# Kernel tuning notes

Hardware: AMD Instinct MI355X
Metric: run time of the kernel (lower is better)

The kernel has to match this reference:

```python
import jax, jax.numpy as jnp
import numpy as np

T, B, I, H, O = 512, 64, 512, 1024, 512
STDV = 1.0 / np.sqrt(H)


def setup_inputs() -> dict:
    key = jax.random.key(0)
    ks = jax.random.split(key, 12)
    u = lambda k, shape: jax.random.uniform(k, shape, jnp.float32, -STDV, STDV)
    return {
        "input": jax.random.normal(ks[0], (T, B, I), jnp.float32),
        "state": jnp.zeros((B, H), jnp.float32),
        "W_zh": u(ks[1], (H, H)), "W_zx": u(ks[2], (I, H)), "b_z": u(ks[3], (H,)),
        "W_rh": u(ks[4], (H, H)), "W_rx": u(ks[5], (I, H)), "b_r": u(ks[6], (H,)),
        "W_hh": u(ks[7], (H, H)), "W_hx": u(ks[8], (I, H)), "b_h": u(ks[9], (H,)),
        "W_out": u(ks[10], (O, H)), "b_out": u(ks[11], (O,)),
    }


def reference(input, state, W_zh, W_zx, b_z, W_rh, W_rx, b_r, W_hh, W_hx, b_h, W_out, b_out):
    # input: [T, B, I]; state: [B, H]
    def step(h, x):
        z = jax.nn.sigmoid(h @ W_zh + x @ W_zx + b_z)
        r = jax.nn.sigmoid(h @ W_rh + x @ W_rx + b_r)
        ht = jnp.tanh((h * r) @ W_hh + x @ W_hx + b_h)
        h = (1.0 - z) * h + z * ht
        y = h @ W_out.T + b_out  # Linear(hidim -> outdim)
        return h, y

    h_final, Y = jax.lax.scan(step, state, input)  # Y: [T, B, O]
    # torch.cat(Y, dim=0) -> [T*B, O]
    return Y.reshape(T * B, O), h_final
```

## Files before the change

kernel.cpp:

```cpp
#include <hip/hip_runtime.h>
#include <cstdint>


#define TT 512
#define BB 64
#define II 512
#define HH 1024
#define OO 512
#define NTHR 512
#define NBLK 512

typedef float4 f4;
__device__ __forceinline__ f4 ld4(const float* p){ return *reinterpret_cast<const f4*>(p); }
__device__ __forceinline__ int swz(int k){ return k ^ (((k >> 4) & 7) << 2); }

__device__ __forceinline__ void ldc16(const float* p, f4* d){
  asm volatile(
    "global_load_dwordx4 %0,  %16, off sc0 sc1\n\t"
    "global_load_dwordx4 %1,  %16, off offset:256 sc0 sc1\n\t"
    "global_load_dwordx4 %2,  %16, off offset:512 sc0 sc1\n\t"
    "global_load_dwordx4 %3,  %16, off offset:768 sc0 sc1\n\t"
    "global_load_dwordx4 %4,  %16, off offset:1024 sc0 sc1\n\t"
    "global_load_dwordx4 %5,  %16, off offset:1280 sc0 sc1\n\t"
    "global_load_dwordx4 %6,  %16, off offset:1536 sc0 sc1\n\t"
    "global_load_dwordx4 %7,  %16, off offset:1792 sc0 sc1\n\t"
    "global_load_dwordx4 %8,  %16, off offset:2048 sc0 sc1\n\t"
    "global_load_dwordx4 %9,  %16, off offset:2304 sc0 sc1\n\t"
    "global_load_dwordx4 %10, %16, off offset:2560 sc0 sc1\n\t"
    "global_load_dwordx4 %11, %16, off offset:2816 sc0 sc1\n\t"
    "global_load_dwordx4 %12, %16, off offset:3072 sc0 sc1\n\t"
    "global_load_dwordx4 %13, %16, off offset:3328 sc0 sc1\n\t"
    "global_load_dwordx4 %14, %16, off offset:3584 sc0 sc1\n\t"
    "s_waitcnt vmcnt(1)\n\t"
    "global_load_dwordx4 %15, %16, off offset:3840 sc0 sc1\n\t"
    "s_waitcnt vmcnt(0)"
    : "=&v"(d[0]),"=&v"(d[1]),"=&v"(d[2]),"=&v"(d[3]),
      "=&v"(d[4]),"=&v"(d[5]),"=&v"(d[6]),"=&v"(d[7]),
      "=&v"(d[8]),"=&v"(d[9]),"=&v"(d[10]),"=&v"(d[11]),
      "=&v"(d[12]),"=&v"(d[13]),"=&v"(d[14]),"=&v"(d[15])
    : "v"(p) : "memory");
}
__device__ __forceinline__ float ldc1(const float* p){
  float v;
  asm volatile("global_load_dword %0, %1, off sc0 sc1\n\ts_waitcnt vmcnt(0)"
               : "=v"(v) : "v"(p) : "memory");
  return v;
}
__device__ __forceinline__ void stc1(float* p, float v){
  asm volatile("global_store_dword %0, %1, off sc0 sc1" :: "v"(p), "v"(v) : "memory");
}

__global__ void k_transpose_x(const float* __restrict__ x, float* __restrict__ xT){
  size_t total = (size_t)TT * II * BB;
  for (size_t n = (size_t)blockIdx.x * blockDim.x + threadIdx.x; n < total;
       n += (size_t)gridDim.x * blockDim.x){
    size_t t = n / ((size_t)II * BB);
    size_t rem = n % ((size_t)II * BB);
    size_t i = rem / BB, b = rem % BB;
    xT[n] = x[(t * BB + b) * II + i];
  }
}

__global__ void k_transpose_wx(const float* __restrict__ W, float* __restrict__ WT){
  size_t n = (size_t)blockIdx.x * blockDim.x + threadIdx.x;
  if (n >= (size_t)II * HH) return;
  size_t j = n / II, k = n % II;
  WT[n] = W[k * HH + j];
}

__global__ void k_transpose_h0(const float* __restrict__ st, float* __restrict__ h0){
  size_t n = (size_t)blockIdx.x * blockDim.x + threadIdx.x;
  if (n >= (size_t)HH * BB) return;
  size_t j = n / BB, b = n % BB;
  h0[n] = st[b * HH + j];
}

__global__ void k_init_bars(unsigned* bars){
  if (threadIdx.x < 1024) bars[threadIdx.x] = 0;
}

__device__ __forceinline__ void g_arrive(unsigned* bars, int g, int jt, unsigned ep){
  asm volatile("s_waitcnt vmcnt(0)" ::: "memory");
  unsigned* leaf = bars + (g * 17 + (jt & 15)) * 16;
  unsigned old = __hip_atomic_fetch_add(leaf, 1u, __ATOMIC_RELAXED, __HIP_MEMORY_SCOPE_AGENT);
  if (old + 1u == ep * 16u)
    __hip_atomic_fetch_add(bars + (g * 17 + 16) * 16, 1u, __ATOMIC_RELAXED, __HIP_MEMORY_SCOPE_AGENT);
}
__device__ __forceinline__ void g_wait(unsigned* bars, int g, unsigned ep){
  unsigned* root = bars + (g * 17 + 16) * 16;
  while (__hip_atomic_load(root, __ATOMIC_RELAXED, __HIP_MEMORY_SCOPE_AGENT) < ep * 16u)
    __builtin_amdgcn_s_sleep(1);
}

#define WREDUCE(v) { v += __shfl_xor(v, 8); v += __shfl_xor(v, 16); v += __shfl_xor(v, 32); }

__global__ __launch_bounds__(NTHR, 2) void k_gru(
    const float* __restrict__ xT,
    const float* __restrict__ WxTr, const float* __restrict__ WxTz, const float* __restrict__ WxTh,
    float* __restrict__ h, float* __restrict__ s,
    const float* __restrict__ W_zh, const float* __restrict__ b_z,
    const float* __restrict__ W_rh, const float* __restrict__ b_r,
    const float* __restrict__ W_hh, const float* __restrict__ b_h,
    const float* __restrict__ W_out, const float* __restrict__ b_out,
    float* __restrict__ out, unsigned* __restrict__ bars)
{
  __shared__ float sW[3 * 4 * 1024];
  __shared__ float red[8 * 272];
  __shared__ float xpre[3][128];
  __shared__ float sZ[128];
  __shared__ float sBias[16];

  const int tid = threadIdx.x;
  const int bid = blockIdx.x;
  const int jt = bid & 255, bhalf = bid >> 8;
  const int j0 = jt * 4, o0 = jt * 2, bbase = bhalf * 32;

  #pragma unroll
  for (int kk2 = 0; kk2 < 2; ++kk2){
    const int k = tid * 2 + kk2;
    f4 vr = ld4(W_rh + (size_t)k * HH + j0);
    f4 vz = ld4(W_zh + (size_t)k * HH + j0);
    f4 vh = ld4(W_hh + (size_t)k * HH + j0);
    const int kx = swz(k);
    float ar[4] = {vr.x,vr.y,vr.z,vr.w};
    float az[4] = {vz.x,vz.y,vz.z,vz.w};
    float ah[4] = {vh.x,vh.y,vh.z,vh.w};
    #pragma unroll
    for (int c = 0; c < 4; ++c){
      sW[0*4096 + c*1024 + kx] = ar[c];
      sW[1*4096 + c*1024 + kx] = az[c];
      sW[2*4096 + c*1024 + kx] = ah[c];
    }
  }
  if (tid < 4){
    sBias[tid]     = b_r[j0 + tid];
    sBias[4 + tid] = b_z[j0 + tid];
    sBias[8 + tid] = b_h[j0 + tid];
    if (tid < 2) sBias[12 + tid] = b_out[o0 + tid];
  }

  const int bg = tid & 7, b0 = bbase + bg * 4;
  const int ksec = tid >> 3;
  const int wv = tid >> 6;
  const bool wr0 = ((tid & 56) == 0);
  const int kh0 = ksec * 16;
  const int kx0 = ksec * 8;
  __syncthreads();

  for (int t = -1; t < TT; ++t){
    f4 st4[16];
    if (t >= 0){
      float aR[4][4] = {};
      ldc16(h + kh0 * BB + b0, st4);
      #pragma unroll
      for (int i4 = 0; i4 < 4; ++i4){
        const int kxc = swz(kh0 + i4*4);
        #pragma unroll
        for (int c = 0; c < 4; ++c){
          f4 wf = *reinterpret_cast<const f4*>(&sW[0*4096 + c*1024 + kxc]);
          float wvv[4] = {wf.x, wf.y, wf.z, wf.w};
          #pragma unroll
          for (int kk = 0; kk < 4; ++kk){
            const f4 hv = st4[i4*4+kk];
            aR[c][0] = fmaf(wvv[kk], hv.x, aR[c][0]);
            aR[c][1] = fmaf(wvv[kk], hv.y, aR[c][1]);
            aR[c][2] = fmaf(wvv[kk], hv.z, aR[c][2]);
            aR[c][3] = fmaf(wvv[kk], hv.w, aR[c][3]);
          }
        }
      }
      #pragma unroll
      for (int c = 0; c < 4; ++c)
        #pragma unroll
        for (int bb = 0; bb < 4; ++bb) WREDUCE(aR[c][bb]);
      if (wr0)
        #pragma unroll
        for (int c = 0; c < 4; ++c)
          #pragma unroll
          for (int bb = 0; bb < 4; ++bb)
            red[wv*272 + c*32 + bg*4 + bb] = aR[c][bb];
      __syncthreads();
      if (tid < 128){
        float sum = 0.f;
        #pragma unroll
        for (int w = 0; w < 8; ++w) sum += red[w*272 + tid];
        const int c = tid >> 5, bl = tid & 31;
        const float v = sum + xpre[0][tid] + sBias[c];
        const float rr = 1.f / (1.f + expf(-v));
        const int jg = j0 + c, bgl = bbase + bl;
        stc1(&s[jg*BB + bgl], rr * ldc1(&h[jg*BB + bgl]));
      }
      __syncthreads();
      if (tid == 0) g_arrive(bars, bhalf, jt, 2*t + 1);

      float aZ[4][4] = {};
      float aY[2][4] = {};
      #pragma unroll
      for (int i4 = 0; i4 < 4; ++i4){
        const int kc = kh0 + i4*4;
        const int kxc = swz(kc);
        #pragma unroll
        for (int c = 0; c < 4; ++c){
          f4 wf = *reinterpret_cast<const f4*>(&sW[1*4096 + c*1024 + kxc]);
          float wvv[4] = {wf.x, wf.y, wf.z, wf.w};
          #pragma unroll
          for (int kk = 0; kk < 4; ++kk){
            const f4 hv = st4[i4*4+kk];
            aZ[c][0] = fmaf(wvv[kk], hv.x, aZ[c][0]);
            aZ[c][1] = fmaf(wvv[kk], hv.y, aZ[c][1]);
            aZ[c][2] = fmaf(wvv[kk], hv.z, aZ[c][2]);
            aZ[c][3] = fmaf(wvv[kk], hv.w, aZ[c][3]);
          }
        }
        #pragma unroll
        for (int oc = 0; oc < 2; ++oc){
          f4 wo = ld4(W_out + (size_t)(o0 + oc) * HH + kc);
          float wvv[4] = {wo.x, wo.y, wo.z, wo.w};
          #pragma unroll
          for (int kk = 0; kk < 4; ++kk){
            const f4 hv = st4[i4*4+kk];
            aY[oc][0] = fmaf(wvv[kk], hv.x, aY[oc][0]);
            aY[oc][1] = fmaf(wvv[kk], hv.y, aY[oc][1]);
            aY[oc][2] = fmaf(wvv[kk], hv.z, aY[oc][2]);
            aY[oc][3] = fmaf(wvv[kk], hv.w, aY[oc][3]);
          }
        }
      }
      #pragma unroll
      for (int c = 0; c < 4; ++c)
        #pragma unroll
        for (int bb = 0; bb < 4; ++bb) WREDUCE(aZ[c][bb]);
      #pragma unroll
      for (int oc = 0; oc < 2; ++oc)
        #pragma unroll
        for (int bb = 0; bb < 4; ++bb) WREDUCE(aY[oc][bb]);
      if (wr0){
        #pragma unroll
        for (int c = 0; c < 4; ++c)
          #pragma unroll
          for (int bb = 0; bb < 4; ++bb)
            red[wv*272 + c*32 + bg*4 + bb] = aZ[c][bb];
        #pragma unroll
        for (int oc = 0; oc < 2; ++oc)
          #pragma unroll
          for (int bb = 0; bb < 4; ++bb)
            red[wv*272 + 128 + oc*32 + bg*4 + bb] = aY[oc][bb];
      }
      __syncthreads();
      if (tid < 128){
        float sum = 0.f;
        #pragma unroll
        for (int w = 0; w < 8; ++w) sum += red[w*272 + tid];
        const int c = tid >> 5;
        sZ[tid] = 1.f / (1.f + expf(-(sum + xpre[1][tid] + sBias[4 + c])));
      } else if (tid < 192){
        const int idx = tid - 128;
        float sum = 0.f;
        #pragma unroll
        for (int w = 0; w < 8; ++w) sum += red[w*272 + tid];
        const int oc = idx >> 5, bl = idx & 31;
        if (t > 0)
          out[((size_t)(t-1)*BB + bbase + bl)*OO + o0 + oc] = sum + sBias[12 + oc];
      }
      if (tid == 0) g_wait(bars, bhalf, 2*t + 1);
      __syncthreads();

      float aH[4][4] = {};
      f4 sv16[16];
      ldc16(s + kh0 * BB + b0, sv16);
      #pragma unroll
      for (int i4 = 0; i4 < 4; ++i4){
        const int kxc = swz(kh0 + i4*4);
        #pragma unroll
        for (int c = 0; c < 4; ++c){
          f4 wf = *reinterpret_cast<const f4*>(&sW[2*4096 + c*1024 + kxc]);
          float wvv[4] = {wf.x, wf.y, wf.z, wf.w};
          #pragma unroll
          for (int kk = 0; kk < 4; ++kk){
            const f4 sv = sv16[i4*4+kk];
            aH[c][0] = fmaf(wvv[kk], sv.x, aH[c][0]);
            aH[c][1] = fmaf(wvv[kk], sv.y, aH[c][1]);
            aH[c][2] = fmaf(wvv[kk], sv.z, aH[c][2]);
            aH[c][3] = fmaf(wvv[kk], sv.w, aH[c][3]);
          }
        }
      }
      #pragma unroll
      for (int c = 0; c < 4; ++c)
        #pragma unroll
        for (int bb = 0; bb < 4; ++bb) WREDUCE(aH[c][bb]);
      if (wr0)
        #pragma unroll
        for (int c = 0; c < 4; ++c)
          #pragma unroll
          for (int bb = 0; bb < 4; ++bb)
            red[wv*272 + c*32 + bg*4 + bb] = aH[c][bb];
      __syncthreads();
      if (tid < 128){
        float sum = 0.f;
        #pragma unroll
        for (int w = 0; w < 8; ++w) sum += red[w*272 + tid];
        const int c = tid >> 5, bl = tid & 31;
        const int jg = j0 + c, bgl = bbase + bl;
        const float ht = tanhf(sum + xpre[2][tid] + sBias[8 + c]);
        const float z = sZ[tid];
        const float hold = ldc1(&h[jg*BB + bgl]);
        const float hnew = fmaf(z, ht - hold, hold);
        stc1(&h[jg*BB + bgl], hnew);
        if (t == TT - 1) out[(size_t)TT*BB*OO + (size_t)bgl*HH + jg] = hnew;
      }
      __syncthreads();
      if (tid == 0) g_arrive(bars, bhalf, jt, 2*t + 2);
    }

    if (t + 1 < TT){
      const int tc = t + 1;
      float aXr[4][4] = {}, aXz[4][4] = {}, aXh[4][4] = {};
      const float* xb = xT + (size_t)tc * II * BB + kx0 * BB + b0;
      #pragma unroll
      for (int i4 = 0; i4 < 2; ++i4){
        f4 xv4[4];
        #pragma unroll
        for (int kk = 0; kk < 4; ++kk) xv4[kk] = ld4(xb + (i4*4+kk) * BB);
        #pragma unroll
        for (int c = 0; c < 4; ++c){
          f4 wr_ = ld4(WxTr + (size_t)(j0 + c) * II + kx0 + i4*4);
          f4 wz_ = ld4(WxTz + (size_t)(j0 + c) * II + kx0 + i4*4);
          f4 wh_ = ld4(WxTh + (size_t)(j0 + c) * II + kx0 + i4*4);
          float wrv[4] = {wr_.x, wr_.y, wr_.z, wr_.w};
          float wzv[4] = {wz_.x, wz_.y, wz_.z, wz_.w};
          float whv[4] = {wh_.x, wh_.y, wh_.z, wh_.w};
          #pragma unroll
          for (int kk = 0; kk < 4; ++kk){
            const f4 xv = xv4[kk];
            aXr[c][0] = fmaf(wrv[kk], xv.x, aXr[c][0]);
            aXr[c][1] = fmaf(wrv[kk], xv.y, aXr[c][1]);
            aXr[c][2] = fmaf(wrv[kk], xv.z, aXr[c][2]);
            aXr[c][3] = fmaf(wrv[kk], xv.w, aXr[c][3]);
            aXz[c][0] = fmaf(wzv[kk], xv.x, aXz[c][0]);
            aXz[c][1] = fmaf(wzv[kk], xv.y, aXz[c][1]);
            aXz[c][2] = fmaf(wzv[kk], xv.z, aXz[c][2]);
            aXz[c][3] = fmaf(wzv[kk], xv.w, aXz[c][3]);
            aXh[c][0] = fmaf(whv[kk], xv.x, aXh[c][0]);
            aXh[c][1] = fmaf(whv[kk], xv.y, aXh[c][1]);
            aXh[c][2] = fmaf(whv[kk], xv.z, aXh[c][2]);
            aXh[c][3] = fmaf(whv[kk], xv.w, aXh[c][3]);
          }
        }
      }
      #pragma unroll
      for (int c = 0; c < 4; ++c)
        #pragma unroll
        for (int bb = 0; bb < 4; ++bb){ WREDUCE(aXr[c][bb]); WREDUCE(aXz[c][bb]); WREDUCE(aXh[c][bb]); }
      if (wr0)
        #pragma unroll
        for (int c = 0; c < 4; ++c)
          #pragma unroll
          for (int bb = 0; bb < 4; ++bb){
            red[wv*272 + c*32 + bg*4 + bb]       = aXr[c][bb];
            red[wv*272 + 128 + c*32 + bg*4 + bb] = aXz[c][bb];
          }
      __syncthreads();
      if (tid < 256){
        float sum = 0.f;
        #pragma unroll
        for (int w = 0; w < 8; ++w) sum += red[w*272 + tid];
        if (tid < 128) xpre[0][tid] = sum;
        else           xpre[1][tid - 128] = sum;
      }
      __syncthreads();
      if (wr0)
        #pragma unroll
        for (int c = 0; c < 4; ++c)
          #pragma unroll
          for (int bb = 0; bb < 4; ++bb)
            red[wv*272 + c*32 + bg*4 + bb] = aXh[c][bb];
      __syncthreads();
      if (tid < 128){
        float sum = 0.f;
        #pragma unroll
        for (int w = 0; w < 8; ++w) sum += red[w*272 + tid];
        xpre[2][tid] = sum;
      }
      __syncthreads();
    }

    if (t >= 0){
      if (tid == 0) g_wait(bars, bhalf, 2*t + 2);
      __syncthreads();
    }
  }

  {
    float aY[2][4] = {};
    f4 hv16[16];
    ldc16(h + kh0 * BB + b0, hv16);
    #pragma unroll
    for (int i4 = 0; i4 < 4; ++i4){
      const int kc = kh0 + i4*4;
      #pragma unroll
      for (int oc = 0; oc < 2; ++oc){
        f4 wo = ld4(W_out + (size_t)(o0 + oc) * HH + kc);
        float wvv[4] = {wo.x, wo.y, wo.z, wo.w};
        #pragma unroll
        for (int kk = 0; kk < 4; ++kk){
          const f4 hv = hv16[i4*4+kk];
          aY[oc][0] = fmaf(wvv[kk], hv.x, aY[oc][0]);
          aY[oc][1] = fmaf(wvv[kk], hv.y, aY[oc][1]);
          aY[oc][2] = fmaf(wvv[kk], hv.z, aY[oc][2]);
          aY[oc][3] = fmaf(wvv[kk], hv.w, aY[oc][3]);
        }
      }
    }
    #pragma unroll
    for (int oc = 0; oc < 2; ++oc)
      #pragma unroll
      for (int bb = 0; bb < 4; ++bb) WREDUCE(aY[oc][bb]);
    if (wr0)
      #pragma unroll
      for (int oc = 0; oc < 2; ++oc)
        #pragma unroll
        for (int bb = 0; bb < 4; ++bb)
          red[wv*272 + oc*32 + bg*4 + bb] = aY[oc][bb];
    __syncthreads();
    if (tid < 64){
      float sum = 0.f;
      #pragma unroll
      for (int w = 0; w < 8; ++w) sum += red[w*272 + tid];
      const int oc = tid >> 5, bl = tid & 31;
      out[((size_t)(TT-1)*BB + bbase + bl)*OO + o0 + oc] = sum + sBias[12 + oc];
    }
  }
}

extern "C" void kernel_launch(void* const* d_in, const int* in_sizes, int n_in,
                              void* d_out, int out_size, void* d_ws, size_t ws_size,
                              hipStream_t stream) {
  const float* x     = (const float*)d_in[0];
  const float* st    = (const float*)d_in[1];
  const float* W_zh  = (const float*)d_in[2];
  const float* W_zx  = (const float*)d_in[3];
  const float* b_z   = (const float*)d_in[4];
  const float* W_rh  = (const float*)d_in[5];
  const float* W_rx  = (const float*)d_in[6];
  const float* b_r   = (const float*)d_in[7];
  const float* W_hh  = (const float*)d_in[8];
  const float* W_hx  = (const float*)d_in[9];
  const float* b_h   = (const float*)d_in[10];
  const float* W_out = (const float*)d_in[11];
  const float* b_out = (const float*)d_in[12];
  float* out = (float*)d_out;
  float* ws  = (float*)d_ws;

  const size_t xT_sz = (size_t)TT * II * BB;
  const size_t wx_sz = (size_t)II * HH;
  const size_t h_sz  = (size_t)HH * BB;
  const size_t need  = (xT_sz + 3*wx_sz + 2*h_sz) * sizeof(float) + 1024*sizeof(unsigned);
  if (ws_size < need) return;

  float* xT   = ws;
  float* WxTr = xT + xT_sz;
  float* WxTz = WxTr + wx_sz;
  float* WxTh = WxTz + wx_sz;
  float* h    = WxTh + wx_sz;
  float* s    = h + h_sz;
  unsigned* bars = (unsigned*)(s + h_sz);

  k_transpose_x <<<8192, 256, 0, stream>>>(x, xT);
  k_transpose_wx<<<2048, 256, 0, stream>>>(W_rx, WxTr);
  k_transpose_wx<<<2048, 256, 0, stream>>>(W_zx, WxTz);
  k_transpose_wx<<<2048, 256, 0, stream>>>(W_hx, WxTh);
  k_transpose_h0<<< 256, 256, 0, stream>>>(st, h);
  k_init_bars   <<<   1, 1024, 0, stream>>>(bars);

  k_gru<<<NBLK, NTHR, 0, stream>>>(xT, WxTr, WxTz, WxTh, h, s,
                                   W_zh, b_z, W_rh, b_r, W_hh, b_h,
                                   W_out, b_out, out, bars);
}
```

Before: 15.05 ms.

## Merge batch halves into one 1024-thread block per hidden tile with single barrier group

Replaces the 512-block, 512-thread grid that split the batch into two halves with 256 blocks of 1024 threads, each covering all 64 batch columns for four hidden units. The two barrier trees collapse into a single grid barrier. The hidden-state loads are streamed in chunks of four instead of holding sixteen vectors, which lowers register pressure, and the input-projection accumulation runs one gate at a time. The aim is to halve the redundant weight staging and barrier traffic per step, at the cost of one block per CU with less latency hiding and a larger shared-memory reduction.

```diff
diff --git a/kernel.cpp b/kernel.cpp
--- a/kernel.cpp
+++ b/kernel.cpp
@@ -7,37 +7,22 @@
 #define II 512
 #define HH 1024
 #define OO 512
-#define NTHR 512
-#define NBLK 512
+#define NTHR 1024
+#define NBLK 256
+#define RSTR 528
 
 typedef float4 f4;
 __device__ __forceinline__ f4 ld4(const float* p){ return *reinterpret_cast<const f4*>(p); }
 __device__ __forceinline__ int swz(int k){ return k ^ (((k >> 4) & 7) << 2); }
 
-__device__ __forceinline__ void ldc16(const float* p, f4* d){
+__device__ __forceinline__ void ldc4(const float* p, f4* d){
   asm volatile(
-    "global_load_dwordx4 %0,  %16, off sc0 sc1\n\t"
-    "global_load_dwordx4 %1,  %16, off offset:256 sc0 sc1\n\t"
-    "global_load_dwordx4 %2,  %16, off offset:512 sc0 sc1\n\t"
-    "global_load_dwordx4 %3,  %16, off offset:768 sc0 sc1\n\t"
-    "global_load_dwordx4 %4,  %16, off offset:1024 sc0 sc1\n\t"
-    "global_load_dwordx4 %5,  %16, off offset:1280 sc0 sc1\n\t"
-    "global_load_dwordx4 %6,  %16, off offset:1536 sc0 sc1\n\t"
-    "global_load_dwordx4 %7,  %16, off offset:1792 sc0 sc1\n\t"
-    "global_load_dwordx4 %8,  %16, off offset:2048 sc0 sc1\n\t"
-    "global_load_dwordx4 %9,  %16, off offset:2304 sc0 sc1\n\t"
-    "global_load_dwordx4 %10, %16, off offset:2560 sc0 sc1\n\t"
-    "global_load_dwordx4 %11, %16, off offset:2816 sc0 sc1\n\t"
-    "global_load_dwordx4 %12, %16, off offset:3072 sc0 sc1\n\t"
-    "global_load_dwordx4 %13, %16, off offset:3328 sc0 sc1\n\t"
-    "global_load_dwordx4 %14, %16, off offset:3584 sc0 sc1\n\t"
-    "s_waitcnt vmcnt(1)\n\t"
-    "global_load_dwordx4 %15, %16, off offset:3840 sc0 sc1\n\t"
+    "global_load_dwordx4 %0, %4, off sc0 sc1\n\t"
+    "global_load_dwordx4 %1, %4, off offset:256 sc0 sc1\n\t"
+    "global_load_dwordx4 %2, %4, off offset:512 sc0 sc1\n\t"
+    "global_load_dwordx4 %3, %4, off offset:768 sc0 sc1\n\t"
     "s_waitcnt vmcnt(0)"
-    : "=&v"(d[0]),"=&v"(d[1]),"=&v"(d[2]),"=&v"(d[3]),
-      "=&v"(d[4]),"=&v"(d[5]),"=&v"(d[6]),"=&v"(d[7]),
-      "=&v"(d[8]),"=&v"(d[9]),"=&v"(d[10]),"=&v"(d[11]),
-      "=&v"(d[12]),"=&v"(d[13]),"=&v"(d[14]),"=&v"(d[15])
+    : "=&v"(d[0]),"=&v"(d[1]),"=&v"(d[2]),"=&v"(d[3])
     : "v"(p) : "memory");
 }
 __device__ __forceinline__ float ldc1(const float* p){
@@ -76,25 +61,24 @@
 }
 
 __global__ void k_init_bars(unsigned* bars){
-  if (threadIdx.x < 1024) bars[threadIdx.x] = 0;
-}
-
-__device__ __forceinline__ void g_arrive(unsigned* bars, int g, int jt, unsigned ep){
+  if (threadIdx.x < 512) bars[threadIdx.x] = 0;
+}
+
+__device__ __forceinline__ void g_arrive(unsigned* bars, int bid, unsigned ep){
   asm volatile("s_waitcnt vmcnt(0)" ::: "memory");
-  unsigned* leaf = bars + (g * 17 + (jt & 15)) * 16;
+  unsigned* leaf = bars + (bid & 15) * 16;
   unsigned old = __hip_atomic_fetch_add(leaf, 1u, __ATOMIC_RELAXED, __HIP_MEMORY_SCOPE_AGENT);
   if (old + 1u == ep * 16u)
-    __hip_atomic_fetch_add(bars + (g * 17 + 16) * 16, 1u, __ATOMIC_RELAXED, __HIP_MEMORY_SCOPE_AGENT);
-}
-__device__ __forceinline__ void g_wait(unsigned* bars, int g, unsigned ep){
-  unsigned* root = bars + (g * 17 + 16) * 16;
-  while (__hip_atomic_load(root, __ATOMIC_RELAXED, __HIP_MEMORY_SCOPE_AGENT) < ep * 16u)
+    __hip_atomic_fetch_add(bars + 256, 1u, __ATOMIC_RELAXED, __HIP_MEMORY_SCOPE_AGENT);
+}
+__device__ __forceinline__ void g_wait(unsigned* bars, unsigned ep){
+  while (__hip_atomic_load(bars + 256, __ATOMIC_RELAXED, __HIP_MEMORY_SCOPE_AGENT) < ep * 16u)
     __builtin_amdgcn_s_sleep(1);
 }
 
-#define WREDUCE(v) { v += __shfl_xor(v, 8); v += __shfl_xor(v, 16); v += __shfl_xor(v, 32); }
-
-__global__ __launch_bounds__(NTHR, 2) void k_gru(
+#define WREDUCE(v) { v += __shfl_xor(v, 16); v += __shfl_xor(v, 32); }
+
+__global__ __launch_bounds__(NTHR) void k_gru(
     const float* __restrict__ xT,
     const float* __restrict__ WxTr, const float* __restrict__ WxTz, const float* __restrict__ WxTh,
     float* __restrict__ h, float* __restrict__ s,
@@ -105,19 +89,17 @@
     float* __restrict__ out, unsigned* __restrict__ bars)
 {
   __shared__ float sW[3 * 4 * 1024];
-  __shared__ float red[8 * 272];
-  __shared__ float xpre[3][128];
-  __shared__ float sZ[128];
+  __shared__ float red[16 * RSTR];
+  __shared__ float xpre[3][256];
+  __shared__ float sZ[256];
   __shared__ float sBias[16];
 
   const int tid = threadIdx.x;
   const int bid = blockIdx.x;
-  const int jt = bid & 255, bhalf = bid >> 8;
-  const int j0 = jt * 4, o0 = jt * 2, bbase = bhalf * 32;
-
-  #pragma unroll
-  for (int kk2 = 0; kk2 < 2; ++kk2){
-    const int k = tid * 2 + kk2;
+  const int j0 = bid * 4, o0 = bid * 2;
+
+  {
+    const int k = tid;
     f4 vr = ld4(W_rh + (size_t)k * HH + j0);
     f4 vz = ld4(W_zh + (size_t)k * HH + j0);
     f4 vh = ld4(W_hh + (size_t)k * HH + j0);
@@ -139,264 +121,253 @@
     if (tid < 2) sBias[12 + tid] = b_out[o0 + tid];
   }
 
-  const int bg = tid & 7, b0 = bbase + bg * 4;
-  const int ksec = tid >> 3;
+  const int bg = tid & 15, b0 = bg * 4;
+  const int ksec = tid >> 4;
   const int wv = tid >> 6;
-  const bool wr0 = ((tid & 56) == 0);
+  const bool wr0 = ((tid & 48) == 0);
   const int kh0 = ksec * 16;
   const int kx0 = ksec * 8;
   __syncthreads();
 
   for (int t = -1; t < TT; ++t){
-    f4 st4[16];
     if (t >= 0){
-      float aR[4][4] = {};
-      ldc16(h + kh0 * BB + b0, st4);
-      #pragma unroll
-      for (int i4 = 0; i4 < 4; ++i4){
-        const int kxc = swz(kh0 + i4*4);
-        #pragma unroll
-        for (int c = 0; c < 4; ++c){
-          f4 wf = *reinterpret_cast<const f4*>(&sW[0*4096 + c*1024 + kxc]);
-          float wvv[4] = {wf.x, wf.y, wf.z, wf.w};
-          #pragma unroll
-          for (int kk = 0; kk < 4; ++kk){
-            const f4 hv = st4[i4*4+kk];
-            aR[c][0] = fmaf(wvv[kk], hv.x, aR[c][0]);
-            aR[c][1] = fmaf(wvv[kk], hv.y, aR[c][1]);
-            aR[c][2] = fmaf(wvv[kk], hv.z, aR[c][2]);
-            aR[c][3] = fmaf(wvv[kk], hv.w, aR[c][3]);
+      const float* hb = h + kh0 * BB + b0;
+
+      {
+        float aR[4][4] = {};
+        #pragma unroll
+        for (int i4 = 0; i4 < 4; ++i4){
+          f4 hv4[4];
+          ldc4(hb + i4*4*BB, hv4);
+          const int kxc = swz(kh0 + i4*4);
+          #pragma unroll
+          for (int c = 0; c < 4; ++c){
+            f4 wf = *reinterpret_cast<const f4*>(&sW[0*4096 + c*1024 + kxc]);
+            float wvv[4] = {wf.x, wf.y, wf.z, wf.w};
+            #pragma unroll
+            for (int kk = 0; kk < 4; ++kk){
+              const f4 hv = hv4[kk];
+              aR[c][0] = fmaf(wvv[kk], hv.x, aR[c][0]);
+              aR[c][1] = fmaf(wvv[kk], hv.y, aR[c][1]);
+              aR[c][2] = fmaf(wvv[kk], hv.z, aR[c][2]);
+              aR[c][3] = fmaf(wvv[kk], hv.w, aR[c][3]);
+            }
           }
         }
-      }
-      #pragma unroll
-      for (int c = 0; c < 4; ++c)
-        #pragma unroll
-        for (int bb = 0; bb < 4; ++bb) WREDUCE(aR[c][bb]);
-      if (wr0)
         #pragma unroll
         for (int c = 0; c < 4; ++c)
           #pragma unroll
-          for (int bb = 0; bb < 4; ++bb)
-            red[wv*272 + c*32 + bg*4 + bb] = aR[c][bb];
-      __syncthreads();
-      if (tid < 128){
+          for (int bb = 0; bb < 4; ++bb) WREDUCE(aR[c][bb]);
+        if (wr0)
+          #pragma unroll
+          for (int c = 0; c < 4; ++c)
+            #pragma unroll
+            for (int bb = 0; bb < 4; ++bb)
+              red[wv*RSTR + c*64 + b0 + bb] = aR[c][bb];
+      }
+      __syncthreads();
+      if (tid < 256){
         float sum = 0.f;
         #pragma unroll
-        for (int w = 0; w < 8; ++w) sum += red[w*272 + tid];
-        const int c = tid >> 5, bl = tid & 31;
+        for (int w = 0; w < 16; ++w) sum += red[w*RSTR + tid];
+        const int c = tid >> 6, bl = tid & 63;
         const float v = sum + xpre[0][tid] + sBias[c];
         const float rr = 1.f / (1.f + expf(-v));
-        const int jg = j0 + c, bgl = bbase + bl;
-        stc1(&s[jg*BB + bgl], rr * ldc1(&h[jg*BB + bgl]));
-      }
-      __syncthreads();
-      if (tid == 0) g_arrive(bars, bhalf, jt, 2*t + 1);
-
-      float aZ[4][4] = {};
-      float aY[2][4] = {};
-      #pragma unroll
-      for (int i4 = 0; i4 < 4; ++i4){
-        const int kc = kh0 + i4*4;
-        const int kxc = swz(kc);
-        #pragma unroll
-        for (int c = 0; c < 4; ++c){
-          f4 wf = *reinterpret_cast<const f4*>(&sW[1*4096 + c*1024 + kxc]);
-          float wvv[4] = {wf.x, wf.y, wf.z, wf.w};
-          #pragma unroll
-          for (int kk = 0; kk < 4; ++kk){
-            const f4 hv = st4[i4*4+kk];
-            aZ[c][0] = fmaf(wvv[kk], hv.x, aZ[c][0]);
-            aZ[c][1] = fmaf(wvv[kk], hv.y, aZ[c][1]);
-            aZ[c][2] = fmaf(wvv[kk], hv.z, aZ[c][2]);
-            aZ[c][3] = fmaf(wvv[kk], hv.w, aZ[c][3]);
+        const int jg = j0 + c;
+        stc1(&s[jg*BB + bl], rr * ldc1(&h[jg*BB + bl]));
+      }
+      __syncthreads();
+      if (tid == 0) g_arrive(bars, bid, 2*t + 1);
+
+      {
+        float aZ[4][4] = {};
+        float aY[2][4] = {};
+        #pragma unroll
+        for (int i4 = 0; i4 < 4; ++i4){
+          f4 hv4[4];
+          ldc4(hb + i4*4*BB, hv4);
+          const int kc = kh0 + i4*4;
+          const int kxc = swz(kc);
+          #pragma unroll
+          for (int c = 0; c < 4; ++c){
+            f4 wf = *reinterpret_cast<const f4*>(&sW[1*4096 + c*1024 + kxc]);
+            float wvv[4] = {wf.x, wf.y, wf.z, wf.w};
+            #pragma unroll
+            for (int kk = 0; kk < 4; ++kk){
+              const f4 hv = hv4[kk];
+              aZ[c][0] = fmaf(wvv[kk], hv.x, aZ[c][0]);
+              aZ[c][1] = fmaf(wvv[kk], hv.y, aZ[c][1]);
+              aZ[c][2] = fmaf(wvv[kk], hv.z, aZ[c][2]);
+              aZ[c][3] = fmaf(wvv[kk], hv.w, aZ[c][3]);
+            }
           }
-        }
-        #pragma unroll
-        for (int oc = 0; oc < 2; ++oc){
-          f4 wo = ld4(W_out + (size_t)(o0 + oc) * HH + kc);
-          float wvv[4] = {wo.x, wo.y, wo.z, wo.w};
-          #pragma unroll
-          for (int kk = 0; kk < 4; ++kk){
-            const f4 hv = st4[i4*4+kk];
-            aY[oc][0] = fmaf(wvv[kk], hv.x, aY[oc][0]);
-            aY[oc][1] = fmaf(wvv[kk], hv.y, aY[oc][1]);
-            aY[oc][2] = fmaf(wvv[kk], hv.z, aY[oc][2]);
-            aY[oc][3] = fmaf(wvv[kk], hv.w, aY[oc][3]);
+          #pragma unroll
+          for (int oc = 0; oc < 2; ++oc){
+            f4 wo = ld4(W_out + (size_t)(o0 + oc) * HH + kc);
+            float wvv[4] = {wo.x, wo.y, wo.z, wo.w};
+            #pragma unroll
+            for (int kk = 0; kk < 4; ++kk){
+              const f4 hv = hv4[kk];
+              aY[oc][0] = fmaf(wvv[kk], hv.x, aY[oc][0]);
+              aY[oc][1] = fmaf(wvv[kk], hv.y, aY[oc][1]);
+              aY[oc][2] = fmaf(wvv[kk], hv.z, aY[oc][2]);
+              aY[oc][3] = fmaf(wvv[kk], hv.w, aY[oc][3]);
+            }
           }
         }
-      }
-      #pragma unroll
-      for (int c = 0; c < 4; ++c)
-        #pragma unroll
-        for (int bb = 0; bb < 4; ++bb) WREDUCE(aZ[c][bb]);
-      #pragma unroll
-      for (int oc = 0; oc < 2; ++oc)
-        #pragma unroll
-        for (int bb = 0; bb < 4; ++bb) WREDUCE(aY[oc][bb]);
-      if (wr0){
         #pragma unroll
         for (int c = 0; c < 4; ++c)
           #pragma unroll
-          for (int bb = 0; bb < 4; ++bb)
-            red[wv*272 + c*32 + bg*4 + bb] = aZ[c][bb];
+          for (int bb = 0; bb < 4; ++bb) WREDUCE(aZ[c][bb]);
         #pragma unroll
         for (int oc = 0; oc < 2; ++oc)
           #pragma unroll
-          for (int bb = 0; bb < 4; ++bb)
-            red[wv*272 + 128 + oc*32 + bg*4 + bb] = aY[oc][bb];
-      }
-      __syncthreads();
-      if (tid < 128){
+          for (int bb = 0; bb < 4; ++bb) WREDUCE(aY[oc][bb]);
+        if (wr0){
+          #pragma unroll
+          for (int c = 0; c < 4; ++c)
+            #pragma unroll
+            for (int bb = 0; bb < 4; ++bb)
+              red[wv*RSTR + c*64 + b0 + bb] = aZ[c][bb];
+          #pragma unroll
+          for (int oc = 0; oc < 2; ++oc)
+            #pragma unroll
+            for (int bb = 0; bb < 4; ++bb)
+              red[wv*RSTR + 256 + oc*64 + b0 + bb] = aY[oc][bb];
+        }
+      }
+      __syncthreads();
+      if (tid < 256){
         float sum = 0.f;
         #pragma unroll
-        for (int w = 0; w < 8; ++w) sum += red[w*272 + tid];
-        const int c = tid >> 5;
+        for (int w = 0; w < 16; ++w) sum += red[w*RSTR + tid];
+        const int c = tid >> 6;
         sZ[tid] = 1.f / (1.f + expf(-(sum + xpre[1][tid] + sBias[4 + c])));
-      } else if (tid < 192){
-        const int idx = tid - 128;
+      } else if (tid < 384){
+        const int idx = tid - 256;
         float sum = 0.f;
         #pragma unroll
-        for (int w = 0; w < 8; ++w) sum += red[w*272 + tid];
-        const int oc = idx >> 5, bl = idx & 31;
+        for (int w = 0; w < 16; ++w) sum += red[w*RSTR + tid];
+        const int oc = idx >> 6, bl = idx & 63;
         if (t > 0)
-          out[((size_t)(t-1)*BB + bbase + bl)*OO + o0 + oc] = sum + sBias[12 + oc];
-      }
-      if (tid == 0) g_wait(bars, bhalf, 2*t + 1);
-      __syncthreads();
-
-      float aH[4][4] = {};
-      f4 sv16[16];
-      ldc16(s + kh0 * BB + b0, sv16);
-      #pragma unroll
-      for (int i4 = 0; i4 < 4; ++i4){
-        const int kxc = swz(kh0 + i4*4);
-        #pragma unroll
-        for (int c = 0; c < 4; ++c){
-          f4 wf = *reinterpret_cast<const f4*>(&sW[2*4096 + c*1024 + kxc]);
-          float wvv[4] = {wf.x, wf.y, wf.z, wf.w};
-          #pragma unroll
-          for (int kk = 0; kk < 4; ++kk){
-            const f4 sv = sv16[i4*4+kk];
-            aH[c][0] = fmaf(wvv[kk], sv.x, aH[c][0]);
-            aH[c][1] = fmaf(wvv[kk], sv.y, aH[c][1]);
-            aH[c][2] = fmaf(wvv[kk], sv.z, aH[c][2]);
-            aH[c][3] = fmaf(wvv[kk], sv.w, aH[c][3]);
+          out[((size_t)(t-1)*BB + bl)*OO + o0 + oc] = sum + sBias[12 + oc];
+      }
+      if (tid == 0) g_wait(bars, 2*t + 1);
+      __syncthreads();
+
+      {
+        float aH[4][4] = {};
+        const float* sb = s + kh0 * BB + b0;
+        #pragma unroll
+        for (int i4 = 0; i4 < 4; ++i4){
+          f4 sv4[4];
+          ldc4(sb + i4*4*BB, sv4);
+          const int kxc = swz(kh0 + i4*4);
+          #pragma unroll
+          for (int c = 0; c < 4; ++c){
+            f4 wf = *reinterpret_cast<const f4*>(&sW[2*4096 + c*1024 + kxc]);
+            float wvv[4] = {wf.x, wf.y, wf.z, wf.w};
+            #pragma unroll
+            for (int kk = 0; kk < 4; ++kk){
+              const f4 sv = sv4[kk];
+              aH[c][0] = fmaf(wvv[kk], sv.x, aH[c][0]);
+              aH[c][1] = fmaf(wvv[kk], sv.y, aH[c][1]);
+              aH[c][2] = fmaf(wvv[kk], sv.z, aH[c][2]);
+              aH[c][3] = fmaf(wvv[kk], sv.w, aH[c][3]);
+            }
           }
         }
-      }
-      #pragma unroll
-      for (int c = 0; c < 4; ++c)
-        #pragma unroll
-        for (int bb = 0; bb < 4; ++bb) WREDUCE(aH[c][bb]);
-      if (wr0)
         #pragma unroll
         for (int c = 0; c < 4; ++c)
           #pragma unroll
-          for (int bb = 0; bb < 4; ++bb)
-            red[wv*272 + c*32 + bg*4 + bb] = aH[c][bb];
-      __syncthreads();
-      if (tid < 128){
+          for (int bb = 0; bb < 4; ++bb) WREDUCE(aH[c][bb]);
+        if (wr0)
+          #pragma unroll
+          for (int c = 0; c < 4; ++c)
+            #pragma unroll
+            for (int bb = 0; bb < 4; ++bb)
+              red[wv*RSTR + c*64 + b0 + bb] = aH[c][bb];
+      }
+      __syncthreads();
+      if (tid < 256){
         float sum = 0.f;
         #pragma unroll
-        for (int w = 0; w < 8; ++w) sum += red[w*272 + tid];
-        const int c = tid >> 5, bl = tid & 31;
-        const int jg = j0 + c, bgl = bbase + bl;
+        for (int w = 0; w < 16; ++w) sum += red[w*RSTR + tid];
+        const int c = tid >> 6, bl = tid & 63;
+        const int jg = j0 + c;
         const float ht = tanhf(sum + xpre[2][tid] + sBias[8 + c]);
         const float z = sZ[tid];
-        const float hold = ldc1(&h[jg*BB + bgl]);
+        const float hold = ldc1(&h[jg*BB + bl]);
         const float hnew = fmaf(z, ht - hold, hold);
-        stc1(&h[jg*BB + bgl], hnew);
-        if (t == TT - 1) out[(size_t)TT*BB*OO + (size_t)bgl*HH + jg] = hnew;
-      }
-      __syncthreads();
-      if (tid == 0) g_arrive(bars, bhalf, jt, 2*t + 2);
+        stc1(&h[jg*BB + bl], hnew);
+        if (t == TT - 1) out[(size_t)TT*BB*OO + (size_t)bl*HH + jg] = hnew;
+      }
+      __syncthreads();
+      if (tid == 0) g_arrive(bars, bid, 2*t + 2);
     }
 
     if (t + 1 < TT){
       const int tc = t + 1;
-      float aXr[4][4] = {}, aXz[4][4] = {}, aXh[4][4] = {};
       const float* xb = xT + (size_t)tc * II * BB + kx0 * BB + b0;
       #pragma unroll
-      for (int i4 = 0; i4 < 2; ++i4){
-        f4 xv4[4];
-        #pragma unroll
-        for (int kk = 0; kk < 4; ++kk) xv4[kk] = ld4(xb + (i4*4+kk) * BB);
-        #pragma unroll
-        for (int c = 0; c < 4; ++c){
-          f4 wr_ = ld4(WxTr + (size_t)(j0 + c) * II + kx0 + i4*4);
-          f4 wz_ = ld4(WxTz + (size_t)(j0 + c) * II + kx0 + i4*4);
-          f4 wh_ = ld4(WxTh + (size_t)(j0 + c) * II + kx0 + i4*4);
-          float wrv[4] = {wr_.x, wr_.y, wr_.z, wr_.w};
-          float wzv[4] = {wz_.x, wz_.y, wz_.z, wz_.w};
-          float whv[4] = {wh_.x, wh_.y, wh_.z, wh_.w};
-          #pragma unroll
-          for (int kk = 0; kk < 4; ++kk){
-            const f4 xv = xv4[kk];
-            aXr[c][0] = fmaf(wrv[kk], xv.x, aXr[c][0]);
-            aXr[c][1] = fmaf(wrv[kk], xv.y, aXr[c][1]);
-            aXr[c][2] = fmaf(wrv[kk], xv.z, aXr[c][2]);
-            aXr[c][3] = fmaf(wrv[kk], xv.w, aXr[c][3]);
-            aXz[c][0] = fmaf(wzv[kk], xv.x, aXz[c][0]);
-            aXz[c][1] = fmaf(wzv[kk], xv.y, aXz[c][1]);
-            aXz[c][2] = fmaf(wzv[kk], xv.z, aXz[c][2]);
-            aXz[c][3] = fmaf(wzv[kk], xv.w, aXz[c][3]);
-            aXh[c][0] = fmaf(whv[kk], xv.x, aXh[c][0]);
-            aXh[c][1] = fmaf(whv[kk], xv.y, aXh[c][1]);
-            aXh[c][2] = fmaf(whv[kk], xv.z, aXh[c][2]);
-            aXh[c][3] = fmaf(whv[kk], xv.w, aXh[c][3]);
+      for (int g = 0; g < 3; ++g){
+        const float* Wg = (g == 0) ? WxTr : (g == 1) ? WxTz : WxTh;
+        {
+          float aX[4][4] = {};
+          #pragma unroll
+          for (int i4 = 0; i4 < 2; ++i4){
+            f4 xv4[4];
+            #pragma unroll
+            for (int kk = 0; kk < 4; ++kk) xv4[kk] = ld4(xb + (i4*4+kk) * BB);
+            #pragma unroll
+            for (int c = 0; c < 4; ++c){
+              f4 wf = ld4(Wg + (size_t)(j0 + c) * II + kx0 + i4*4);
+              float wvv[4] = {wf.x, wf.y, wf.z, wf.w};
+              #pragma unroll
+              for (int kk = 0; kk < 4; ++kk){
+                const f4 xv = xv4[kk];
+                aX[c][0] = fmaf(wvv[kk], xv.x, aX[c][0]);
+                aX[c][1] = fmaf(wvv[kk], xv.y, aX[c][1]);
+                aX[c][2] = fmaf(wvv[kk], xv.z, aX[c][2]);
+                aX[c][3] = fmaf(wvv[kk], xv.w, aX[c][3]);
+              }
+            }
           }
-        }
-      }
-      #pragma unroll
-      for (int c = 0; c < 4; ++c)
-        #pragma unroll
-        for (int bb = 0; bb < 4; ++bb){ WREDUCE(aXr[c][bb]); WREDUCE(aXz[c][bb]); WREDUCE(aXh[c][bb]); }
-      if (wr0)
-        #pragma unroll
-        for (int c = 0; c < 4; ++c)
-          #pragma unroll
-          for (int bb = 0; bb < 4; ++bb){
-            red[wv*272 + c*32 + bg*4 + bb]       = aXr[c][bb];
-            red[wv*272 + 128 + c*32 + bg*4 + bb] = aXz[c][bb];
-          }
-      __syncthreads();
-      if (tid < 256){
-        float sum = 0.f;
-        #pragma unroll
-        for (int w = 0; w < 8; ++w) sum += red[w*272 + tid];
-        if (tid < 128) xpre[0][tid] = sum;
-        else           xpre[1][tid - 128] = sum;
-      }
-      __syncthreads();
-      if (wr0)
-        #pragma unroll
-        for (int c = 0; c < 4; ++c)
-          #pragma unroll
-          for (int bb = 0; bb < 4; ++bb)
-            red[wv*272 + c*32 + bg*4 + bb] = aXh[c][bb];
-      __syncthreads();
-      if (tid < 128){
-        float sum = 0.f;
-        #pragma unroll
-        for (int w = 0; w < 8; ++w) sum += red[w*272 + tid];
-        xpre[2][tid] = sum;
-      }
-      __syncthreads();
+          #pragma unroll
+          for (int c = 0; c < 4; ++c)
+            #pragma unroll
+            for (int bb = 0; bb < 4; ++bb) WREDUCE(aX[c][bb]);
+          if (wr0)
+            #pragma unroll
+            for (int c = 0; c < 4; ++c)
+              #pragma unroll
+              for (int bb = 0; bb < 4; ++bb)
+                red[wv*RSTR + c*64 + b0 + bb] = aX[c][bb];
+        }
+        __syncthreads();
+        if (tid < 256){
+          float sum = 0.f;
+          #pragma unroll
+          for (int w = 0; w < 16; ++w) sum += red[w*RSTR + tid];
+          xpre[g][tid] = sum;
+        }
+        __syncthreads();
+      }
     }
 
     if (t >= 0){
-      if (tid == 0) g_wait(bars, bhalf, 2*t + 2);
+      if (tid == 0) g_wait(bars, 2*t + 2);
       __syncthreads();
     }
   }
 
   {
     float aY[2][4] = {};
-    f4 hv16[16];
-    ldc16(h + kh0 * BB + b0, hv16);
+    const float* hb = h + kh0 * BB + b0;
     #pragma unroll
     for (int i4 = 0; i4 < 4; ++i4){
+      f4 hv4[4];
+      ldc4(hb + i4*4*BB, hv4);
       const int kc = kh0 + i4*4;
       #pragma unroll
       for (int oc = 0; oc < 2; ++oc){
@@ -404,7 +375,7 @@
         float wvv[4] = {wo.x, wo.y, wo.z, wo.w};
         #pragma unroll
         for (int kk = 0; kk < 4; ++kk){
-          const f4 hv = hv16[i4*4+kk];
+          const f4 hv = hv4[kk];
           aY[oc][0] = fmaf(wvv[kk], hv.x, aY[oc][0]);
           aY[oc][1] = fmaf(wvv[kk], hv.y, aY[oc][1]);
           aY[oc][2] = fmaf(wvv[kk], hv.z, aY[oc][2]);
@@ -421,14 +392,14 @@
       for (int oc = 0; oc < 2; ++oc)
         #pragma unroll
         for (int bb = 0; bb < 4; ++bb)
-          red[wv*272 + oc*32 + bg*4 + bb] = aY[oc][bb];
+          red[wv*RSTR + oc*64 + b0 + bb] = aY[oc][bb];
     __syncthreads();
-    if (tid < 64){
+    if (tid < 128){
       float sum = 0.f;
       #pragma unroll
-      for (int w = 0; w < 8; ++w) sum += red[w*272 + tid];
-      const int oc = tid >> 5, bl = tid & 31;
-      out[((size_t)(TT-1)*BB + bbase + bl)*OO + o0 + oc] = sum + sBias[12 + oc];
+      for (int w = 0; w < 16; ++w) sum += red[w*RSTR + tid];
+      const int oc = tid >> 6, bl = tid & 63;
+      out[((size_t)(TT-1)*BB + bl)*OO + o0 + oc] = sum + sBias[12 + oc];
     }
   }
 }
@@ -455,7 +426,7 @@
   const size_t xT_sz = (size_t)TT * II * BB;
   const size_t wx_sz = (size_t)II * HH;
   const size_t h_sz  = (size_t)HH * BB;
-  const size_t need  = (xT_sz + 3*wx_sz + 2*h_sz) * sizeof(float) + 1024*sizeof(unsigned);
+  const size_t need  = (xT_sz + 3*wx_sz + 2*h_sz) * sizeof(float) + 512*sizeof(unsigned);
   if (ws_size < need) return;
 
   float* xT   = ws;
@@ -471,7 +442,7 @@
   k_transpose_wx<<<2048, 256, 0, stream>>>(W_zx, WxTz);
   k_transpose_wx<<<2048, 256, 0, stream>>>(W_hx, WxTh);
   k_transpose_h0<<< 256, 256, 0, stream>>>(st, h);
-  k_init_bars   <<<   1, 1024, 0, stream>>>(bars);
+  k_init_bars   <<<   1, 512, 0, stream>>>(bars);
 
   k_gru<<<NBLK, NTHR, 0, stream>>>(xT, WxTr, WxTz, WxTh, h, s,
                                    W_zh, b_z, W_rh, b_r, W_hh, b_h,
```

Measured after the change: 15.19 ms. Within noise of the previous version (+0.9%).
